# Kernel optimization log

Hardware: AMD Instinct MI355X
Metric: run time of the kernel (lower is better)

The kernel has to match this reference:

```python
import jax, jax.numpy as jnp
import numpy as np

B, D, T = 32, 1024, 1000
LMAX = 200
VOCAB = 80
BLANK = VOCAB - 1
NEG = -1e30


def setup_inputs() -> dict:
    key = jax.random.key(0)
    ks = jax.random.split(key, 8)
    decoder_outputs = jax.random.normal(ks[0], (B, D, T), dtype=jnp.float32)
    target_text = jax.random.randint(ks[1], (B, LMAX), 0, BLANK, dtype=jnp.int32)
    decoder_lengths = jax.random.randint(ks[2], (B,), T // 2, T + 1, dtype=jnp.int32)
    target_lengths = jax.random.randint(ks[3], (B,), 1, LMAX + 1, dtype=jnp.int32)
    # learned params (dropout is identity in eval / deterministic reference)
    W1 = jax.random.normal(ks[4], (D, D), dtype=jnp.float32) * (1.0 / np.sqrt(D))
    b1 = jnp.zeros((D,), dtype=jnp.float32)
    W2 = jax.random.normal(ks[5], (D, VOCAB), dtype=jnp.float32) * (1.0 / np.sqrt(D))
    b2 = jnp.zeros((VOCAB,), dtype=jnp.float32)
    return {"decoder_outputs": decoder_outputs, "target_text": target_text,
            "decoder_lengths": decoder_lengths, "target_lengths": target_lengths,
            "W1": W1, "b1": b1, "W2": W2, "b2": b2}


def _ctc_nll(log_probs, targets, input_lengths, target_lengths):
    # log_probs: [T, B, V]; standard CTC alpha (forward) DP over extended labels.
    Tt, Bb, V = log_probs.shape
    L = targets.shape[1]
    S = 2 * L + 1
    ext = jnp.full((Bb, S), BLANK, dtype=targets.dtype).at[:, 1::2].set(targets)
    ext_m2 = jnp.pad(ext, ((0, 0), (2, 0)), constant_values=BLANK)[:, :S]
    allow_skip = (ext != BLANK) & (ext != ext_m2)
    allow_skip = allow_skip.at[:, :2].set(False)

    lp0 = log_probs[0]  # [B, V]
    alpha0 = jnp.full((Bb, S), NEG, dtype=log_probs.dtype)
    alpha0 = alpha0.at[:, 0].set(lp0[:, BLANK])
    alpha0 = alpha0.at[:, 1].set(jnp.take_along_axis(lp0, targets[:, :1], axis=1)[:, 0])

    def step(alpha, inp):
        lp_t, t = inp
        emit = jnp.take_along_axis(lp_t, ext, axis=1)  # [B, S]
        a2 = jnp.pad(alpha, ((0, 0), (1, 0)), constant_values=NEG)[:, :S]
        a3 = jnp.pad(alpha, ((0, 0), (2, 0)), constant_values=NEG)[:, :S]
        a3 = jnp.where(allow_skip, a3, NEG)
        new = jnp.logaddexp(jnp.logaddexp(alpha, a2), a3) + emit
        alpha = jnp.where((t < input_lengths)[:, None], new, alpha)
        return alpha, None

    alpha, _ = jax.lax.scan(step, alpha0, (log_probs[1:], jnp.arange(1, Tt)))
    i1 = (2 * target_lengths - 1)[:, None]
    i2 = (2 * target_lengths)[:, None]
    last = jnp.logaddexp(jnp.take_along_axis(alpha, i1, axis=1)[:, 0],
                         jnp.take_along_axis(alpha, i2, axis=1)[:, 0])
    nll = -last
    # zero_infinity=True: invalid alignments -> 0 loss
    return jnp.where(last > NEG / 2, nll, 0.0)


def reference(decoder_outputs, target_text, decoder_lengths, target_lengths, W1, b1, W2, b2):
    x = jnp.transpose(decoder_outputs, (0, 2, 1))          # [B, T, D]
    h = jax.nn.relu(jnp.einsum('btd,de->bte', x, W1) + b1)  # proj + ReLU (dropout=identity)
    logits = jnp.einsum('btd,dv->btv', h, W2) + b2          # [B, T, V]
    log_probs = jax.nn.log_softmax(logits, axis=2)
    log_probs = jnp.transpose(log_probs, (1, 0, 2))         # [T, B, V]
    ctc_loss = _ctc_nll(log_probs, target_text, decoder_lengths, target_lengths)
    return (ctc_loss / decoder_lengths.astype(jnp.float32)).mean()
```

## Files before the change

### kernel.cpp

```cpp
#include <hip/hip_runtime.h>
#include <cstdint>
#include <cstddef>

#define BN_ 32
#define DD_ 1024
#define TT_ 1000
#define LMAX_ 200
#define VC_ 80
#define BLANK_ 79
#define SS_ 401
#define SPAD 512
#define NEGV (-1e30f)

typedef _Float16 half8 __attribute__((ext_vector_type(8)));
typedef float f32x4 __attribute__((ext_vector_type(4)));

__device__ __forceinline__ void async16(const void* g, void* l) {
  __builtin_amdgcn_global_load_lds(
      (const __attribute__((address_space(1))) unsigned int*)g,
      (__attribute__((address_space(3))) unsigned int*)l, 16, 0, 0);
}

__global__ __launch_bounds__(256) void transpose_all_kernel(
    const float* __restrict__ dec, const float* __restrict__ W1,
    const float* __restrict__ W2, _Float16* __restrict__ Af,
    _Float16* __restrict__ W1T, _Float16* __restrict__ W2T) {
  __shared__ _Float16 T[64][72];
  int z = blockIdx.z;
  const float* in; _Float16* out; int C;
  const int R = 1024;
  if (z < 32) {
    in = dec + (size_t)z * R * TT_;
    out = Af + (size_t)z * TT_ * R;
    C = TT_;
  } else if (z == 32) {
    in = W1; out = W1T; C = 1024;
  } else {
    in = W2; out = W2T; C = VC_;
  }
  int c0 = blockIdx.x * 64, r0 = blockIdx.y * 64;
  if (c0 >= C) return;
  int tid = threadIdx.x;
  int cl = tid & 63, rg = tid >> 6;
  int c = c0 + cl;
  bool cv = (c < C);
  const float* ip = in + (size_t)(r0 + rg * 16) * C + c;
  _Float16 h[16];
#pragma unroll
  for (int i = 0; i < 16; ++i) h[i] = cv ? (_Float16)ip[(size_t)i * C] : (_Float16)0.f;
  *(half8*)&T[cl][rg * 16] = *(half8*)&h[0];
  *(half8*)&T[cl][rg * 16 + 8] = *(half8*)&h[8];
  __syncthreads();
  int cr = tid >> 2, rc = (tid & 3) * 16;
  if (c0 + cr < C) {
    half8 a = *(const half8*)&T[cr][rc];
    half8 b2 = *(const half8*)&T[cr][rc + 8];
    _Float16* op = out + (size_t)(c0 + cr) * R + r0 + rc;
    *(half8*)op = a;
    *(half8*)(op + 8) = b2;
  }
}

__device__ __forceinline__ void stage_half(const _Float16* __restrict__ X,
                                           int x0, int kt, int h,
                                           _Float16* lds, int tid, int K) {
#pragma unroll
  for (int jj = 0; jj < 2; ++jj) {
    int seg = tid + 512 * jj;
    int row = seg >> 3, slot = seg & 7;
    int cg = slot ^ (row & 7);
    async16(X + (size_t)(x0 + h * 128 + row) * K + kt * 64 + cg * 8,
            lds + seg * 8);
  }
}

__global__ __launch_bounds__(512, 2) void gemm_relu_kernel(
    const _Float16* __restrict__ A, const _Float16* __restrict__ Bt,
    const float* __restrict__ bias, _Float16* __restrict__ H,
    int M, int N, int K) {
  __shared__ __align__(16) _Float16 sA[2][16384];
  __shared__ __align__(16) _Float16 sB[2][16384];
  int tid = threadIdx.x;
  int wave = tid >> 6, lane = tid & 63;
  int quad = lane >> 4, r16 = lane & 15;
  int wm = wave >> 2, wn = wave & 3;

  int orig = blockIdx.x, nwg = gridDim.x;
  int xcd = orig & 7, loc = orig >> 3;
  int qq = nwg >> 3, rr = nwg & 7;
  int wg = (xcd < rr ? xcd * (qq + 1) : rr * (qq + 1) + (xcd - rr) * qq) + loc;
  int m0 = (wg >> 2) * 256, n0 = (wg & 3) * 256;

  f32x4 acc[4][8];
#pragma unroll
  for (int q = 0; q < 4; ++q)
#pragma unroll
    for (int f = 0; f < 8; ++f) acc[q][f] = {0.f, 0.f, 0.f, 0.f};

  stage_half(A, m0, 0, 0, &sA[0][0], tid, K);
  stage_half(A, m0, 0, 1, &sA[0][8192], tid, K);
  stage_half(Bt, n0, 0, 0, &sB[0][0], tid, K);
  stage_half(Bt, n0, 0, 1, &sB[0][8192], tid, K);
  stage_half(A, m0, 1, 0, &sA[1][0], tid, K);
  stage_half(Bt, n0, 1, 0, &sB[1][0], tid, K);
  stage_half(A, m0, 1, 1, &sA[1][8192], tid, K);
  asm volatile("s_waitcnt vmcnt(6)" ::: "memory");
  __builtin_amdgcn_s_barrier();

  const int NKT = K >> 6;
#pragma unroll 2
  for (int t = 0; t < NKT; ++t) {
    int cur = t & 1, nxt = cur ^ 1;
    int t1 = (t + 1 < NKT) ? t + 1 : NKT - 1;
    int t2 = (t + 2 < NKT) ? t + 2 : NKT - 1;
    const _Float16* As = sA[cur];
    const _Float16* Bs = sB[cur];
#pragma unroll
    for (int q = 0; q < 4; ++q) {
      const int qm = q >> 1, qn = q & 1;
      half8 af[4][2], bf[2][2];
      int abase = (qm * 128 + wm * 64 + r16) * 64;
      int bbase = (qn * 128 + wn * 32 + r16) * 64;
      int sw0 = ((0 * 4 + quad) ^ (r16 & 7)) * 8;
      int sw1 = ((1 * 4 + quad) ^ (r16 & 7)) * 8;
#pragma unroll
      for (int i = 0; i < 4; ++i) {
        af[i][0] = *(const half8*)&As[abase + i * 16 * 64 + sw0];
        af[i][1] = *(const half8*)&As[abase + i * 16 * 64 + sw1];
      }
#pragma unroll
      for (int j = 0; j < 2; ++j) {
        bf[j][0] = *(const half8*)&Bs[bbase + j * 16 * 64 + sw0];
        bf[j][1] = *(const half8*)&Bs[bbase + j * 16 * 64 + sw1];
      }
      if (q == 0) stage_half(Bt, n0, t1, 1, &sB[nxt][8192], tid, K);
      else if (q == 1) stage_half(A, m0, t2, 0, &sA[cur][0], tid, K);
      else if (q == 2) stage_half(Bt, n0, t2, 0, &sB[cur][0], tid, K);
      else stage_half(A, m0, t2, 1, &sA[cur][8192], tid, K);
      __builtin_amdgcn_s_barrier();
      asm volatile("s_waitcnt lgkmcnt(0)" ::: "memory");
      __builtin_amdgcn_s_setprio(1);
#pragma unroll
      for (int i = 0; i < 4; ++i)
#pragma unroll
        for (int j = 0; j < 2; ++j) {
          acc[q][i * 2 + j] = __builtin_amdgcn_mfma_f32_16x16x32_f16(
              af[i][0], bf[j][0], acc[q][i * 2 + j], 0, 0, 0);
          acc[q][i * 2 + j] = __builtin_amdgcn_mfma_f32_16x16x32_f16(
              af[i][1], bf[j][1], acc[q][i * 2 + j], 0, 0, 0);
        }
      __builtin_amdgcn_s_setprio(0);
      if (q == 3) asm volatile("s_waitcnt vmcnt(6)" ::: "memory");
      __builtin_amdgcn_s_barrier();
    }
  }
  asm volatile("s_waitcnt vmcnt(0)" ::: "memory");

  float bvv[2][2];
#pragma unroll
  for (int qn = 0; qn < 2; ++qn)
#pragma unroll
    for (int j = 0; j < 2; ++j)
      bvv[qn][j] = bias[n0 + qn * 128 + wn * 32 + j * 16 + r16];
#pragma unroll
  for (int q = 0; q < 4; ++q) {
    const int qm = q >> 1, qn = q & 1;
#pragma unroll
    for (int i = 0; i < 4; ++i)
#pragma unroll
      for (int j = 0; j < 2; ++j) {
#pragma unroll
        for (int r = 0; r < 4; ++r) {
          int m = m0 + qm * 128 + wm * 64 + i * 16 + quad * 4 + r;
          int n = n0 + qn * 128 + wn * 32 + j * 16 + r16;
          float v = acc[q][i * 2 + j][r] + bvv[qn][j];
          H[(size_t)m * N + n] = (_Float16)fmaxf(v, 0.f);
        }
      }
  }
}

__global__ __launch_bounds__(256) void gemm_prob_kernel(
    const _Float16* __restrict__ A, const _Float16* __restrict__ Bt,
    const float* __restrict__ bias, float* __restrict__ P, int M, int K) {
  constexpr int BK = 64;
  __shared__ __align__(16) _Float16 sA[64 * BK];
  __shared__ __align__(16) _Float16 sB[VC_ * BK];
  int tid = threadIdx.x;
  int wave = tid >> 6, lane = tid & 63;
  int quad = lane >> 4, r16 = lane & 15;
  int m0 = blockIdx.x * 64;

  f32x4 acc[5];
#pragma unroll
  for (int j = 0; j < 5; ++j) acc[j] = {0.f, 0.f, 0.f, 0.f};

  for (int kt = 0; kt < K; kt += BK) {
#pragma unroll
    for (int jj = 0; jj < 2; ++jj) {
      int seg = tid + 256 * jj;
      int row = seg >> 3, slot = seg & 7;
      int cg = slot ^ (row & 7);
      async16(A + (size_t)(m0 + row) * K + kt + cg * 8, &sA[seg * 8]);
    }
#pragma unroll
    for (int jj = 0; jj < 3; ++jj) {
      int seg = tid + 256 * jj;
      if (seg < VC_ * 8) {
        int row = seg >> 3, slot = seg & 7;
        int cg = slot ^ (row & 7);
        async16(Bt + (size_t)row * K + kt + cg * 8, &sB[seg * 8]);
      }
    }
    __syncthreads();
#pragma unroll
    for (int ku = 0; ku < 2; ++ku) {
      int sw = ((ku * 4 + quad) ^ (r16 & 7)) * 8;
      half8 af = *(const half8*)&sA[(wave * 16 + r16) * BK + sw];
      half8 bfr[5];
#pragma unroll
      for (int j = 0; j < 5; ++j)
        bfr[j] = *(const half8*)&sB[(j * 16 + r16) * BK + sw];
#pragma unroll
      for (int j = 0; j < 5; ++j)
        acc[j] = __builtin_amdgcn_mfma_f32_16x16x32_f16(af, bfr[j], acc[j], 0, 0, 0);
    }
    __syncthreads();
  }
  float bv[5];
#pragma unroll
  for (int j = 0; j < 5; ++j) bv[j] = bias[j * 16 + r16];
#pragma unroll
  for (int rr = 0; rr < 4; ++rr) {
    float vals[5];
    float mx = -3.4e38f;
#pragma unroll
    for (int j = 0; j < 5; ++j) {
      vals[j] = acc[j][rr] + bv[j];
      mx = fmaxf(mx, vals[j]);
    }
#pragma unroll
    for (int d = 1; d < 16; d <<= 1) mx = fmaxf(mx, __shfl_xor(mx, d));
    float ex[5], sm = 0.f;
#pragma unroll
    for (int j = 0; j < 5; ++j) { ex[j] = __expf(vals[j] - mx); sm += ex[j]; }
#pragma unroll
    for (int d = 1; d < 16; d <<= 1) sm += __shfl_xor(sm, d);
    float rinv = 1.f / sm;
    int m = m0 + wave * 16 + quad * 4 + rr;
    float* o = P + (size_t)m * VC_;
#pragma unroll
    for (int j = 0; j < 5; ++j) o[j * 16 + r16] = ex[j] * rinv;
  }
}

__global__ __launch_bounds__(256) void emit_kernel(
    const float* __restrict__ P, const int* __restrict__ targets,
    float* __restrict__ EM) {
  int idx = blockIdx.x * 256 + threadIdx.x;
  int s = idx & (SPAD - 1);
  int bt = idx >> 9;
  float v = 0.f;
  if (s < SS_) {
    int lab = BLANK_;
    if (s & 1) {
      int b = bt / TT_;
      lab = targets[b * LMAX_ + (s >> 1)];
    }
    v = P[(size_t)bt * VC_ + lab];
  }
  EM[idx] = v;
}

__device__ __forceinline__ void dp_step_fwd(float (&bta)[8], int& k,
                                            const f32x4 e0, const f32x4 e1,
                                            const float (&am)[4], int lane) {
  float pm1 = __shfl_up(bta[7], 1);
  int pk = __shfl_up(k, 1);
  if (lane == 0) { pm1 = 0.f; pk = k; }
  int knew = max(k, pk);
  pm1 = ldexpf(pm1, pk - knew);
  int ds = k - knew;
#pragma unroll
  for (int r = 0; r < 8; ++r) bta[r] = ldexpf(bta[r], ds);
  k = knew;
  float nb[8];
  nb[0] = (bta[0] + pm1) * e0.x;
  nb[1] = fmaf(am[0], pm1, bta[1] + bta[0]) * e0.y;
  nb[2] = (bta[2] + bta[1]) * e0.z;
  nb[3] = fmaf(am[1], bta[1], bta[3] + bta[2]) * e0.w;
  nb[4] = (bta[4] + bta[3]) * e1.x;
  nb[5] = fmaf(am[2], bta[3], bta[5] + bta[4]) * e1.y;
  nb[6] = (bta[6] + bta[5]) * e1.z;
  nb[7] = fmaf(am[3], bta[5], bta[7] + bta[6]) * e1.w;
#pragma unroll
  for (int r = 0; r < 8; ++r) bta[r] = nb[r];
}

__device__ __forceinline__ void dp_step_bwd(float (&g)[8], int& k,
                                            const f32x4 e0, const f32x4 e1,
                                            const float (&amB)[4], int lane) {
  float gh[8];
  gh[0] = g[0] * e0.x; gh[1] = g[1] * e0.y;
  gh[2] = g[2] * e0.z; gh[3] = g[3] * e0.w;
  gh[4] = g[4] * e1.x; gh[5] = g[5] * e1.y;
  gh[6] = g[6] * e1.z; gh[7] = g[7] * e1.w;
  float qm1 = __shfl_down(gh[0], 1);
  float qm2 = __shfl_down(gh[1], 1);
  int nk = __shfl_down(k, 1);
  if (lane == 63) { qm1 = 0.f; qm2 = 0.f; nk = k; }
  int knew = max(k, nk);
  int dq = nk - knew;
  qm1 = ldexpf(qm1, dq);
  qm2 = ldexpf(qm2, dq);
  int ds = k - knew;
#pragma unroll
  for (int r = 0; r < 8; ++r) gh[r] = ldexpf(gh[r], ds);
  k = knew;
  g[0] = gh[0] + gh[1];
  g[1] = fmaf(amB[0], gh[3], gh[1] + gh[2]);
  g[2] = gh[2] + gh[3];
  g[3] = fmaf(amB[1], gh[5], gh[3] + gh[4]);
  g[4] = gh[4] + gh[5];
  g[5] = fmaf(amB[2], gh[7], gh[5] + gh[6]);
  g[6] = gh[6] + gh[7];
  g[7] = fmaf(amB[3], qm2, gh[7] + qm1);
}

__device__ __forceinline__ void dp_rescale(float (&v)[8], int& k) {
  float m = fmaxf(fmaxf(fmaxf(v[0], v[1]), fmaxf(v[2], v[3])),
                  fmaxf(fmaxf(v[4], v[5]), fmaxf(v[6], v[7])));
  int ex = (__float_as_int(m) >> 23) - 126;
  k += ex;
#pragma unroll
  for (int r = 0; r < 8; ++r) v[r] = ldexpf(v[r], -ex);
}

__device__ __forceinline__ float allow_f(const int* __restrict__ tg, int s) {
  if (!(s & 1) || s < 3) return 0.f;
  int li = s >> 1;
  if (li >= LMAX_) return 0.f;
  int lab = tg[li];
  return (lab != BLANK_ && lab != tg[li - 1]) ? 1.f : 0.f;
}

__global__ __launch_bounds__(128) void ctc_dp_kernel(
    const float* __restrict__ EM, const int* __restrict__ targets,
    const int* __restrict__ dlen, const int* __restrict__ tlen,
    float* __restrict__ out) {
  __shared__ float sg[SPAD];
  __shared__ int skg[64];
  int b = blockIdx.x;
  int wave = threadIdx.x >> 6;
  int lane = threadIdx.x & 63;
  const float* em = EM + (size_t)b * TT_ * SPAD + lane * 8;
  const int* tg = targets + b * LMAX_;
  int Tl = dlen[b], Ll = tlen[b];
  int tm = Tl >> 1;

  constexpr int PD = 8;
  f32x4 pf[PD][2];
  float v[8];
  int k = 0;

  if (wave == 0) {
    float am[4];
#pragma unroll
    for (int j = 0; j < 4; ++j) am[j] = allow_f(tg, lane * 8 + 2 * j + 1);
    f32x4 r0a = *(const f32x4*)(em);
#pragma unroll
    for (int r = 0; r < 8; ++r) v[r] = 0.f;
    if (lane == 0) { v[0] = r0a.x; v[1] = r0a.y; }
#pragma unroll
    for (int j = 0; j < PD; ++j) {
      int ri = min(1 + j, TT_ - 1);
      pf[j][0] = *(const f32x4*)(em + (size_t)ri * SPAD);
      pf[j][1] = *(const f32x4*)(em + (size_t)ri * SPAD + 4);
    }
    int t = 1;
    for (; t + (PD - 1) <= tm; t += PD) {
#pragma unroll
      for (int u = 0; u < PD; ++u) {
        dp_step_fwd(v, k, pf[u][0], pf[u][1], am, lane);
        if (u & 1) dp_rescale(v, k);
        int ri = min(t + u + PD, TT_ - 1);
        pf[u][0] = *(const f32x4*)(em + (size_t)ri * SPAD);
        pf[u][1] = *(const f32x4*)(em + (size_t)ri * SPAD + 4);
      }
    }
#pragma unroll
    for (int u = 0; u < PD; ++u) {
      if (t + u <= tm) {
        dp_step_fwd(v, k, pf[u][0], pf[u][1], am, lane);
        if (u & 1) dp_rescale(v, k);
      }
    }
  } else {
    float amB[4];
#pragma unroll
    for (int j = 0; j < 4; ++j) amB[j] = allow_f(tg, lane * 8 + 2 * j + 3);
    int s1 = 2 * Ll - 1, s2 = 2 * Ll;
#pragma unroll
    for (int r = 0; r < 8; ++r) {
      int s = lane * 8 + r;
      v[r] = (s == s1 || s == s2) ? 1.f : 0.f;
    }
#pragma unroll
    for (int j = 0; j < PD; ++j) {
      int ri = max(Tl - 1 - j, 0);
      pf[j][0] = *(const f32x4*)(em + (size_t)ri * SPAD);
      pf[j][1] = *(const f32x4*)(em + (size_t)ri * SPAD + 4);
    }
    int t = Tl - 1;
    for (; t - (PD - 1) > tm; t -= PD) {
#pragma unroll
      for (int u = 0; u < PD; ++u) {
        dp_step_bwd(v, k, pf[u][0], pf[u][1], amB, lane);
        if (u & 1) dp_rescale(v, k);
        int ri = max(t - u - PD, 0);
        pf[u][0] = *(const f32x4*)(em + (size_t)ri * SPAD);
        pf[u][1] = *(const f32x4*)(em + (size_t)ri * SPAD + 4);
      }
    }
#pragma unroll
    for (int u = 0; u < PD; ++u) {
      if (t - u > tm) {
        dp_step_bwd(v, k, pf[u][0], pf[u][1], amB, lane);
        if (u & 1) dp_rescale(v, k);
      }
    }
#pragma unroll
    for (int r = 0; r < 8; ++r) sg[lane * 8 + r] = v[r];
    skg[lane] = k;
  }
  __syncthreads();
  if (wave == 0) {
    float p = 0.f;
#pragma unroll
    for (int r = 0; r < 8; ++r) p = fmaf(v[r], sg[lane * 8 + r], p);
    int kk = k + skg[lane];
    if (p == 0.f) kk = -(1 << 30);
#pragma unroll
    for (int d = 1; d < 64; d <<= 1) {
      float po = __shfl_xor(p, d);
      int ko = __shfl_xor(kk, d);
      int km = max(kk, ko);
      p = ldexpf(p, kk - km) + ldexpf(po, ko - km);
      kk = km;
    }
    if (lane == 0) {
      float nll = 0.f;
      if (p > 0.f) nll = -((log2f(p) + (float)kk) * 0.69314718055994531f);
      atomicAdd(out, nll / (float)Tl * (1.f / BN_));
    }
  }
}

extern "C" void kernel_launch(void* const* d_in, const int* in_sizes, int n_in,
                              void* d_out, int out_size, void* d_ws, size_t ws_size,
                              hipStream_t stream) {
  const float* dec = (const float*)d_in[0];
  const int* tgt   = (const int*)d_in[1];
  const int* dln   = (const int*)d_in[2];
  const int* tln   = (const int*)d_in[3];
  const float* W1  = (const float*)d_in[4];
  const float* b1  = (const float*)d_in[5];
  const float* W2  = (const float*)d_in[6];
  const float* b2  = (const float*)d_in[7];
  float* out = (float*)d_out;

  char* ws = (char*)d_ws;
  const size_t M = (size_t)BN_ * TT_;
  _Float16* Af   = (_Float16*)(ws);
  float* EM      = (float*)(ws);
  _Float16* Hf   = (_Float16*)(ws + 65536000);
  _Float16* W1T  = (_Float16*)(ws + 131072000);
  _Float16* W2T  = (_Float16*)(ws + 133169152);
  float* Pp      = (float*)(ws + 133332992);

  hipMemsetAsync(d_out, 0, sizeof(float), stream);

  transpose_all_kernel<<<dim3(16, 16, 34), 256, 0, stream>>>(
      dec, W1, W2, Af, W1T, W2T);
  gemm_relu_kernel<<<dim3((1024 / 256) * (M / 256), 1, 1), 512, 0, stream>>>(
      Af, W1T, b1, Hf, (int)M, DD_, DD_);
  gemm_prob_kernel<<<dim3(M / 64, 1, 1), 256, 0, stream>>>(
      Hf, W2T, b2, Pp, (int)M, DD_);
  emit_kernel<<<dim3((BN_ * TT_ * SPAD) / 256, 1, 1), 256, 0, stream>>>(Pp, tgt, EM);
  ctc_dp_kernel<<<dim3(BN_, 1, 1), 128, 0, stream>>>(EM, tgt, dln, tln, out);
}
```

Baseline: 418.6 us.

## Restructure GEMM inner loop into k-split phases with reordered async staging

Reorganizes each K-tile's compute from four output quadrants into four phases split by M-half and k-subtile, so B fragments are loaded from LDS once per k-subtile and reused across both M halves. The prefetch schedule for the global-to-LDS async copies is changed to match: one A half of the next tile is staged at phase 0 and three halves of tile t+2 at phase 3, with the vmcnt waits adjusted to match. This aims to cut LDS read traffic and better overlap loads with MFMA, but changes buffer-hazard timing and register pressure, which risks data races or reduced occupancy.

Measured after the change: 419.5 us. Within noise of the previous version (+0.2%).

```diff
diff --git a/kernel.cpp b/kernel.cpp
--- a/kernel.cpp
+++ b/kernel.cpp
@@ -103,7 +103,7 @@
   stage_half(Bt, n0, 0, 1, &sB[0][8192], tid, K);
   stage_half(A, m0, 1, 0, &sA[1][0], tid, K);
   stage_half(Bt, n0, 1, 0, &sB[1][0], tid, K);
-  stage_half(A, m0, 1, 1, &sA[1][8192], tid, K);
+  stage_half(Bt, n0, 1, 1, &sB[1][8192], tid, K);
   asm volatile("s_waitcnt vmcnt(6)" ::: "memory");
   __builtin_amdgcn_s_barrier();
 
@@ -115,42 +115,46 @@
     int t2 = (t + 2 < NKT) ? t + 2 : NKT - 1;
     const _Float16* As = sA[cur];
     const _Float16* Bs = sB[cur];
-#pragma unroll
-    for (int q = 0; q < 4; ++q) {
-      const int qm = q >> 1, qn = q & 1;
-      half8 af[4][2], bf[2][2];
+    half8 bf[2][2];
+#pragma unroll
+    for (int ph = 0; ph < 4; ++ph) {
+      const int qm = ph & 1;
+      const int ku = ph >> 1;
+      const bool loadB = (qm == 0);
+      int sw = ((ku * 4 + quad) ^ (r16 & 7)) * 8;
+      half8 af[4];
       int abase = (qm * 128 + wm * 64 + r16) * 64;
-      int bbase = (qn * 128 + wn * 32 + r16) * 64;
-      int sw0 = ((0 * 4 + quad) ^ (r16 & 7)) * 8;
-      int sw1 = ((1 * 4 + quad) ^ (r16 & 7)) * 8;
-#pragma unroll
-      for (int i = 0; i < 4; ++i) {
-        af[i][0] = *(const half8*)&As[abase + i * 16 * 64 + sw0];
-        af[i][1] = *(const half8*)&As[abase + i * 16 * 64 + sw1];
-      }
-#pragma unroll
-      for (int j = 0; j < 2; ++j) {
-        bf[j][0] = *(const half8*)&Bs[bbase + j * 16 * 64 + sw0];
-        bf[j][1] = *(const half8*)&Bs[bbase + j * 16 * 64 + sw1];
-      }
-      if (q == 0) stage_half(Bt, n0, t1, 1, &sB[nxt][8192], tid, K);
-      else if (q == 1) stage_half(A, m0, t2, 0, &sA[cur][0], tid, K);
-      else if (q == 2) stage_half(Bt, n0, t2, 0, &sB[cur][0], tid, K);
-      else stage_half(A, m0, t2, 1, &sA[cur][8192], tid, K);
+#pragma unroll
+      for (int i = 0; i < 4; ++i)
+        af[i] = *(const half8*)&As[abase + i * 16 * 64 + sw];
+      if (loadB) {
+#pragma unroll
+        for (int qn = 0; qn < 2; ++qn)
+#pragma unroll
+          for (int j = 0; j < 2; ++j)
+            bf[qn][j] = *(const half8*)&Bs[(qn * 128 + wn * 32 + j * 16 + r16) * 64 + sw];
+      }
+      if (ph == 0) {
+        stage_half(A, m0, t1, 1, &sA[nxt][8192], tid, K);
+      } else if (ph == 3) {
+        stage_half(A, m0, t2, 0, &sA[cur][0], tid, K);
+        stage_half(Bt, n0, t2, 0, &sB[cur][0], tid, K);
+        stage_half(Bt, n0, t2, 1, &sB[cur][8192], tid, K);
+      }
       __builtin_amdgcn_s_barrier();
       asm volatile("s_waitcnt lgkmcnt(0)" ::: "memory");
       __builtin_amdgcn_s_setprio(1);
 #pragma unroll
-      for (int i = 0; i < 4; ++i)
-#pragma unroll
-        for (int j = 0; j < 2; ++j) {
-          acc[q][i * 2 + j] = __builtin_amdgcn_mfma_f32_16x16x32_f16(
-              af[i][0], bf[j][0], acc[q][i * 2 + j], 0, 0, 0);
-          acc[q][i * 2 + j] = __builtin_amdgcn_mfma_f32_16x16x32_f16(
-              af[i][1], bf[j][1], acc[q][i * 2 + j], 0, 0, 0);
-        }
+      for (int qn = 0; qn < 2; ++qn)
+#pragma unroll
+        for (int i = 0; i < 4; ++i)
+#pragma unroll
+          for (int j = 0; j < 2; ++j)
+            acc[qm * 2 + qn][i * 2 + j] = __builtin_amdgcn_mfma_f32_16x16x32_f16(
+                af[i], bf[qn][j], acc[qm * 2 + qn][i * 2 + j], 0, 0, 0);
       __builtin_amdgcn_s_setprio(0);
-      if (q == 3) asm volatile("s_waitcnt vmcnt(6)" ::: "memory");
+      if (ph == 0 || ph == 3)
+        asm volatile("s_waitcnt vmcnt(8)" ::: "memory");
       __builtin_amdgcn_s_barrier();
     }
   }
```
